# Optimization experiments

Hardware: AMD Instinct MI355X
Metric: run time of the kernel (lower is better)

## Reference

```python
import jax, jax.numpy as jnp
import numpy as np

B, S, E, H, W, HID, V, OUT, L = 2, 2048, 512, 8, 5, 2048, 32000, 6, 6
DH = E // H
SCALE = DH ** -0.5
PAD = (W - 1) // 2
SK = S - W + 1  # number of k/v windows from torch unfold


def setup_inputs() -> dict:
    key = jax.random.key(0)
    ks = jax.random.split(key, 16)
    def g(i, shape, s):
        return jax.random.normal(ks[i], shape, jnp.float32) * s
    return {
        "inputs": jax.random.randint(ks[0], (B, S), 0, V),
        "emb": g(1, (V, E), 0.02),
        "ln_w": jnp.ones((E,), jnp.float32),
        "ln_b": jnp.zeros((E,), jnp.float32),
        "q_w": g(2, (E, E), E ** -0.5), "q_b": jnp.zeros((E,), jnp.float32),
        "k_w": g(3, (E, E), E ** -0.5), "k_b": jnp.zeros((E,), jnp.float32),
        "v_w": g(4, (E, E), E ** -0.5), "v_b": jnp.zeros((E,), jnp.float32),
        "fc1_w": g(5, (E, HID), E ** -0.5), "fc1_b": jnp.zeros((HID,), jnp.float32),
        "fc2_w": g(6, (HID, E), HID ** -0.5), "fc2_b": jnp.zeros((E,), jnp.float32),
        "out_w": g(7, (E * S, OUT), (E * S) ** -0.5), "out_b": jnp.zeros((OUT,), jnp.float32),
    }


def _pos_encoding():
    pos = jnp.arange(S, dtype=jnp.float32)[:, None]
    div = jnp.exp(jnp.arange(0, E, 2, dtype=jnp.float32) * (-np.log(10000.0) / E))
    pe = jnp.zeros((S, E), jnp.float32)
    pe = pe.at[:, 0::2].set(jnp.sin(pos * div)).at[:, 1::2].set(jnp.cos(pos * div))
    return pe


def reference(inputs, emb, ln_w, ln_b, q_w, q_b, k_w, k_b, v_w, v_b,
              fc1_w, fc1_b, fc2_w, fc2_b, out_w, out_b):
    x = emb[inputs] + _pos_encoding()  # [B,S,E]

    def ln(t):
        m = t.mean(-1, keepdims=True)
        v_ = t.var(-1, keepdims=True)
        return (t - m) / jnp.sqrt(v_ + 1e-5) * ln_w + ln_b

    def attn(x):
        def heads(w, b):
            return (x @ w + b).reshape(B, S, H, DH).transpose(0, 2, 1, 3)  # [B,H,S,dh]
        q, k, v = heads(q_w, q_b), heads(k_w, k_b), heads(v_w, v_b)
        qp = jnp.pad(q, ((0, 0), (0, 0), (PAD, PAD), (0, 0)))  # [B,H,S+W-1,dh]
        # torch unfold -> windows [..., dh, W]; einsum contracts dh AND W, so flatten both.
        q_un = jnp.stack([qp[:, :, j:j + S, :] for j in range(W)], axis=-1).reshape(B, H, S, DH * W)
        k_un = jnp.stack([k[:, :, j:j + SK, :] for j in range(W)], axis=-1).reshape(B, H, SK, DH * W)
        scores = jnp.einsum('bhqf,bhkf->bhqk', q_un, k_un) * SCALE  # [B,H,S,SK]
        a = jax.nn.softmax(scores, axis=-1)
        # output einsum 'bnqk,bnkdh->bnqd' sums attn-weighted v over k AND window dim;
        # since attn is independent of window pos, presum v over the window.
        v_sum = sum(v[:, :, j:j + SK, :] for j in range(W))  # [B,H,SK,dh]
        o = jnp.einsum('bhqk,bhkd->bhqd', a, v_sum)
        return o.transpose(0, 2, 1, 3).reshape(B, S, E)

    for _ in range(L):
        x = ln(attn(x))
        x = (jax.nn.relu(x @ fc1_w + fc1_b) @ fc2_w + fc2_b) + x
        x = ln(x)
    return x.reshape(B, -1) @ out_w + out_b  # [B,OUT]
```

## Files before the change

kernel.cpp:

```cpp
#include <hip/hip_runtime.h>
#include <math.h>


namespace {
constexpr int kB   = 2;
constexpr int kS   = 2048;
constexpr int kE   = 512;
constexpr int kH   = 8;
constexpr int kDH  = 64;
constexpr int kSK  = 2044;
constexpr int kHID = 2048;
constexpr int kL   = 6;
constexpr float kScaleL2 = 0.125f * 1.44269504088896f;
constexpr int kTok = kB * kS;
constexpr int kNX  = kTok * kE;
constexpr int kQKV = 3 * kE;
constexpr int kSQ  = 72;
constexpr int kSV  = 136;
}

using f16x8   = __attribute__((ext_vector_type(8))) _Float16;
using floatx4 = __attribute__((ext_vector_type(4))) float;
using uint2v  = __attribute__((ext_vector_type(2))) unsigned int;
using uint4v  = __attribute__((ext_vector_type(4))) unsigned int;

static __device__ __forceinline__ unsigned short f2h(float f) {
  return __builtin_bit_cast(unsigned short, (_Float16)f);
}
static __device__ __forceinline__ float h2f(unsigned short u) {
  return (float)__builtin_bit_cast(_Float16, u);
}
static __device__ __forceinline__ unsigned int pk2h(float a, float b) {
  return __builtin_bit_cast(unsigned int, __builtin_amdgcn_cvt_pkrtz(a, b));
}
static __device__ __forceinline__ float red16(float x, bool hi) {
  const unsigned u = __builtin_bit_cast(unsigned, x);
  const uint2v r = __builtin_amdgcn_permlane16_swap(u, u, false, false);
  return __builtin_bit_cast(float, hi ? r[0] : r[1]);
}
static __device__ __forceinline__ float red32(float x, bool hi) {
  const unsigned u = __builtin_bit_cast(unsigned, x);
  const uint2v r = __builtin_amdgcn_permlane32_swap(u, u, false, false);
  return __builtin_bit_cast(float, hi ? r[0] : r[1]);
}

__global__ __launch_bounds__(256) void embed_kernel(const int* __restrict__ idx,
        const float* __restrict__ emb, unsigned short* __restrict__ X) {
  const int bs  = blockIdx.x;
  const int s   = bs & (kS - 1);
  const int tok = idx[bs];
  const int t   = threadIdx.x;
#pragma unroll
  for (int r = 0; r < 2; ++r) {
    const int e = t + 256 * r;
    const int i = e >> 1;
    const float dv  = __expf((float)(2 * i) * (-9.210340371976184f / (float)kE));
    const float ang = (float)s * dv;
    const float pe  = (e & 1) ? cosf(ang) : sinf(ang);
    X[bs * kE + e] = f2h(emb[tok * kE + e] + pe);
  }
}

__global__ __launch_bounds__(256) void tcast_kernel(const float* __restrict__ src,
        unsigned short* __restrict__ dst, int K, int N) {
  __shared__ float t[32][33];
  const int tid = threadIdx.x;
  const int tx = tid & 31, ty = tid >> 5;
  const int n0 = blockIdx.x * 32, k0 = blockIdx.y * 32;
#pragma unroll
  for (int p = 0; p < 4; ++p)
    t[ty + 8 * p][tx] = src[(size_t)(k0 + ty + 8 * p) * N + n0 + tx];
  __syncthreads();
#pragma unroll
  for (int p = 0; p < 4; ++p)
    dst[(size_t)(n0 + ty + 8 * p) * K + k0 + tx] = f2h(t[tx][ty + 8 * p]);
}

__global__ __launch_bounds__(256) void qkvb_kernel(const float* __restrict__ qb,
        const float* __restrict__ kb, const float* __restrict__ vb,
        float* __restrict__ dst) {
  const int i = blockIdx.x * 256 + threadIdx.x;
  dst[i] = (i < 512) ? qb[i] : ((i < 1024) ? kb[i - 512] : vb[i - 1024]);
}

template <int RELU, int RES>
__global__ __launch_bounds__(256) void mfma_gemm(const unsigned short* __restrict__ A,
        const unsigned short* __restrict__ Bt, const float* __restrict__ bias,
        const unsigned short* __restrict__ Rm, unsigned short* __restrict__ C,
        int M, int N, int K) {
  __shared__ __align__(16) unsigned short As[128 * 40];
  __shared__ __align__(16) unsigned short Bs[128 * 40];
  const int tid = threadIdx.x;
  const int m0 = blockIdx.y * 128, n0 = blockIdx.x * 128;
  const int wid = tid >> 6, lane = tid & 63;
  const int lm = lane & 15, quad = lane >> 4;
  const int wm = (wid & 1) * 64, wn = (wid >> 1) * 64;
  const int bn = tid >> 2, bk = (tid & 3) * 8;
  floatx4 acc[4][4] = {};
  for (int k0 = 0; k0 < K; k0 += 32) {
#pragma unroll
    for (int p = 0; p < 2; ++p) {
      const uint4 va = *(const uint4*)&A[(size_t)(m0 + bn + 64 * p) * K + k0 + bk];
      *(uint4*)&As[(bn + 64 * p) * 40 + bk] = va;
      const uint4 vb = *(const uint4*)&Bt[(size_t)(n0 + bn + 64 * p) * K + k0 + bk];
      *(uint4*)&Bs[(bn + 64 * p) * 40 + bk] = vb;
    }
    __syncthreads();
    f16x8 af[4], bf[4];
#pragma unroll
    for (int t = 0; t < 4; ++t) {
      af[t] = *(const f16x8*)&As[(wm + t * 16 + lm) * 40 + quad * 8];
      bf[t] = *(const f16x8*)&Bs[(wn + t * 16 + lm) * 40 + quad * 8];
    }
#pragma unroll
    for (int mt = 0; mt < 4; ++mt)
#pragma unroll
      for (int nt = 0; nt < 4; ++nt)
        acc[mt][nt] = __builtin_amdgcn_mfma_f32_16x16x32_f16(
            af[mt], bf[nt], acc[mt][nt], 0, 0, 0);
    __syncthreads();
  }
#pragma unroll
  for (int mt = 0; mt < 4; ++mt) {
#pragma unroll
    for (int nt = 0; nt < 4; ++nt) {
      const int n = n0 + wn + nt * 16 + lm;
      const float bv = bias[n];
#pragma unroll
      for (int r = 0; r < 4; ++r) {
        const int m = m0 + wm + mt * 16 + quad * 4 + r;
        float o = acc[mt][nt][r] + bv;
        if (RES) o += h2f(Rm[(size_t)m * N + n]);
        if (RELU) o = fmaxf(o, 0.f);
        C[(size_t)m * N + n] = f2h(o);
      }
    }
  }
}

__global__ __launch_bounds__(256) void vsumt_kernel(const unsigned short* __restrict__ QKVh,
        unsigned short* __restrict__ VsT) {
  const int t0 = blockIdx.x * 64;
  const int h = blockIdx.y, b = blockIdx.z;
  const int tid = threadIdx.x;
  __shared__ float Ls[68 * 65];
  for (int id = tid; id < 68 * 8; id += 256) {
    const int row = id >> 3, d8 = (id & 7) * 8;
    const int gt = t0 + row;
    float v[8];
    if (gt < kS) {
      const unsigned short* p =
          &QKVh[(size_t)(b * kS + gt) * kQKV + 2 * kE + h * kDH + d8];
      const ushort4 a = *(const ushort4*)p;
      const ushort4 c = *(const ushort4*)(p + 4);
      v[0] = h2f(a.x); v[1] = h2f(a.y); v[2] = h2f(a.z); v[3] = h2f(a.w);
      v[4] = h2f(c.x); v[5] = h2f(c.y); v[6] = h2f(c.z); v[7] = h2f(c.w);
    } else {
#pragma unroll
      for (int j = 0; j < 8; ++j) v[j] = 0.f;
    }
#pragma unroll
    for (int j = 0; j < 8; ++j) Ls[row * 65 + d8 + j] = v[j];
  }
  __syncthreads();
  const int t4 = (tid & 15) * 4;
#pragma unroll
  for (int c = 0; c < 4; ++c) {
    const int d = (tid >> 4) + 16 * c;
    ushort4 o;
    unsigned short* op = (unsigned short*)&o;
#pragma unroll
    for (int j = 0; j < 4; ++j) {
      const int tl = t4 + j;
      float s = Ls[(tl + 0) * 65 + d] + Ls[(tl + 1) * 65 + d]
              + Ls[(tl + 2) * 65 + d] + Ls[(tl + 3) * 65 + d]
              + Ls[(tl + 4) * 65 + d];
      if (t0 + tl >= kSK) s = 0.f;
      op[j] = f2h(s);
    }
    *(ushort4*)&VsT[((size_t)(b * kH + h) * kDH + d) * (size_t)kS + t0 + t4] = o;
  }
}

__global__ __launch_bounds__(512) void flash_kernel(const unsigned short* __restrict__ QKVh,
        const unsigned short* __restrict__ VsT, unsigned short* __restrict__ O) {
  const int tid = threadIdx.x;
  const int qt = blockIdx.x, h = blockIdx.y, b = blockIdx.z;
  const int q0 = qt * 64;
  const int wid = tid >> 6, lane = tid & 63;
  const int lm = lane & 15, quad = lane >> 4;
  const bool h16 = (lane & 16) != 0, h32 = (lane & 32) != 0;
  const int wq = wid >> 2, wt = wid & 3;
  const int bh = b * kH + h;

  __shared__ __align__(16) unsigned short Qs[68 * kSQ];
  __shared__ __align__(16) unsigned short Ks[132 * kSQ];
  __shared__ __align__(16) unsigned short Vt[64 * kSV];
  __shared__ float mM[64][4], lM[64][4];

  for (int id = tid; id < 68 * 16; id += 512) {
    const int row = id >> 4, c4 = (id & 15) * 4;
    const int gq = q0 - 2 + row;
    ushort4 v = make_ushort4(0, 0, 0, 0);
    if (gq >= 0 && gq < kS)
      v = *(const ushort4*)&QKVh[(size_t)(b * kS + gq) * kQKV + h * kDH + c4];
    *(ushort4*)&Qs[row * kSQ + c4] = v;
  }

  const int prow = tid >> 4;
  const int pc4 = (tid & 15) * 4, pc8 = (tid & 15) * 8;
  ushort4 kreg[5];
  uint4 vreg[2];
#define PREFETCH(T0)                                                          \
  {                                                                           \
    _Pragma("unroll")                                                         \
    for (int p = 0; p < 5; ++p) {                                             \
      const int row = prow + 32 * p;                                          \
      ushort4 v = make_ushort4(0, 0, 0, 0);                                   \
      if (row < 132) {                                                        \
        const int gk = (T0) + row;                                            \
        if (gk < kS)                                                          \
          v = *(const ushort4*)&QKVh[(size_t)(b * kS + gk) * kQKV + kE +      \
                                     h * kDH + pc4];                          \
      }                                                                       \
      kreg[p] = v;                                                            \
    }                                                                         \
    _Pragma("unroll")                                                         \
    for (int p = 0; p < 2; ++p)                                               \
      vreg[p] = *(const uint4*)&VsT[((size_t)bh * kDH + prow + 32 * p) *      \
                                    (size_t)kS + (T0) + pc8];                 \
  }
  PREFETCH(0)

  float mrow[2], lrow[2];
  mrow[0] = mrow[1] = -1e30f;
  lrow[0] = lrow[1] = 0.f;
  floatx4 Oacc[2][4] = {};
  const int asrc = (lane >> 2) & 12;

  for (int t0 = 0; t0 < kSK; t0 += 128) {
    __syncthreads();
#pragma unroll
    for (int p = 0; p < 5; ++p) {
      const int row = prow + 32 * p;
      if (row < 132) *(ushort4*)&Ks[row * kSQ + pc4] = kreg[p];
    }
#pragma unroll
    for (int p = 0; p < 2; ++p)
      *(uint4*)&Vt[(prow + 32 * p) * kSV + pc8] = vreg[p];
    __syncthreads();
    const int tn = t0 + 128;
    if (tn < kSK) PREFETCH(tn)

    floatx4 sac[2][2] = {};
    __builtin_amdgcn_s_setprio(1);
#pragma unroll
    for (int kk = 0; kk < 10; ++kk) {
      const int w = kk >> 1, d0 = (kk & 1) * 32;
      const f16x8 kf0 = *(const f16x8*)&Ks[(wt * 32 + lm + w) * kSQ + d0 + quad * 8];
      const f16x8 kf1 = *(const f16x8*)&Ks[(wt * 32 + 16 + lm + w) * kSQ + d0 + quad * 8];
      const f16x8 qf0 = *(const f16x8*)&Qs[(wq * 32 + lm + w) * kSQ + d0 + quad * 8];
      const f16x8 qf1 = *(const f16x8*)&Qs[(wq * 32 + 16 + lm + w) * kSQ + d0 + quad * 8];
      sac[0][0] = __builtin_amdgcn_mfma_f32_16x16x32_f16(kf0, qf0, sac[0][0], 0, 0, 0);
      sac[0][1] = __builtin_amdgcn_mfma_f32_16x16x32_f16(kf0, qf1, sac[0][1], 0, 0, 0);
      sac[1][0] = __builtin_amdgcn_mfma_f32_16x16x32_f16(kf1, qf0, sac[1][0], 0, 0, 0);
      sac[1][1] = __builtin_amdgcn_mfma_f32_16x16x32_f16(kf1, qf1, sac[1][1], 0, 0, 0);
    }
    __builtin_amdgcn_s_setprio(0);

    if (t0 + wt * 32 + 32 > kSK) {
#pragma unroll
      for (int tf = 0; tf < 2; ++tf)
#pragma unroll
        for (int r = 0; r < 4; ++r) {
          const int tg = t0 + wt * 32 + tf * 16 + quad * 4 + r;
          if (tg >= kSK) { sac[tf][0][r] = -1e30f; sac[tf][1][r] = -1e30f; }
        }
    }

    float alpha_q[2];
    f16x8 pfrag[2];
#pragma unroll
    for (int qf = 0; qf < 2; ++qf) {
      float mx = fmaxf(
          fmaxf(fmaxf(sac[0][qf][0], sac[0][qf][1]), fmaxf(sac[0][qf][2], sac[0][qf][3])),
          fmaxf(fmaxf(sac[1][qf][0], sac[1][qf][1]), fmaxf(sac[1][qf][2], sac[1][qf][3])));
      mx = fmaxf(mx, red16(mx, h16));
      mx = fmaxf(mx, red32(mx, h32));
      const float mnew = fmaxf(mrow[qf], mx * kScaleL2);
      const float al = exp2f(mrow[qf] - mnew);
      float e[2][4];
#pragma unroll
      for (int tf = 0; tf < 2; ++tf)
#pragma unroll
        for (int r = 0; r < 4; ++r)
          e[tf][r] = exp2f(fmaf(sac[tf][qf][r], kScaleL2, -mnew));
      float ps = ((e[0][0] + e[0][1]) + (e[0][2] + e[0][3]))
               + ((e[1][0] + e[1][1]) + (e[1][2] + e[1][3]));
      ps += red16(ps, h16);
      ps += red32(ps, h32);
      lrow[qf] = lrow[qf] * al + ps;
      mrow[qf] = mnew;
      alpha_q[qf] = al;
      const unsigned w00 = pk2h(e[0][0], e[0][1]);
      const unsigned w01 = pk2h(e[0][2], e[0][3]);
      const unsigned w10 = pk2h(e[1][0], e[1][1]);
      const unsigned w11 = pk2h(e[1][2], e[1][3]);
      const uint2v sA = __builtin_amdgcn_permlane32_swap(w00, w10, false, false);
      const uint2v dA = __builtin_amdgcn_permlane16_swap(sA[0], sA[1], false, false);
      const uint2v sB = __builtin_amdgcn_permlane32_swap(w01, w11, false, false);
      const uint2v dB = __builtin_amdgcn_permlane16_swap(sB[0], sB[1], false, false);
      uint4v fr;
      fr[0] = dA[0]; fr[1] = dB[0]; fr[2] = dA[1]; fr[3] = dB[1];
      pfrag[qf] = __builtin_bit_cast(f16x8, fr);
    }
    float alpha_o[2][4];
#pragma unroll
    for (int qf = 0; qf < 2; ++qf)
#pragma unroll
      for (int r = 0; r < 4; ++r)
        alpha_o[qf][r] = __shfl(alpha_q[qf], asrc + r);
#pragma unroll
    for (int ms = 0; ms < 2; ++ms)
#pragma unroll
      for (int nt2 = 0; nt2 < 4; ++nt2)
#pragma unroll
        for (int r = 0; r < 4; ++r)
          Oacc[ms][nt2][r] *= alpha_o[ms][r];
    {
      const int tcol = wt * 32 + quad * 8;
      __builtin_amdgcn_s_setprio(1);
#pragma unroll
      for (int nt2 = 0; nt2 < 4; ++nt2) {
        const f16x8 vf = *(const f16x8*)&Vt[(nt2 * 16 + lm) * kSV + tcol];
        Oacc[0][nt2] = __builtin_amdgcn_mfma_f32_16x16x32_f16(pfrag[0], vf, Oacc[0][nt2], 0, 0, 0);
        Oacc[1][nt2] = __builtin_amdgcn_mfma_f32_16x16x32_f16(pfrag[1], vf, Oacc[1][nt2], 0, 0, 0);
      }
      __builtin_amdgcn_s_setprio(0);
    }
  }
  if (quad == 0) {
#pragma unroll
    for (int qf = 0; qf < 2; ++qf) {
      const int row = wq * 32 + qf * 16 + lm;
      mM[row][wt] = mrow[qf];
      lM[row][wt] = lrow[qf];
    }
  }
  __syncthreads();
  float fac[2][4], invL[2][4];
#pragma unroll
  for (int qf = 0; qf < 2; ++qf)
#pragma unroll
    for (int r = 0; r < 4; ++r) {
      const int row = wq * 32 + qf * 16 + quad * 4 + r;
      const float M = fmaxf(fmaxf(mM[row][0], mM[row][1]),
                            fmaxf(mM[row][2], mM[row][3]));
      const float L = lM[row][0] * exp2f(mM[row][0] - M)
                    + lM[row][1] * exp2f(mM[row][1] - M)
                    + lM[row][2] * exp2f(mM[row][2] - M)
                    + lM[row][3] * exp2f(mM[row][3] - M);
      fac[qf][r] = exp2f(mM[row][wt] - M);
      invL[qf][r] = 1.f / L;
    }
  float* OfA = (float*)Vt;
  float* OfB = (float*)Ks;
  if (!(wt & 1)) {
    float* Of = (wt == 0) ? OfA : OfB;
#pragma unroll
    for (int ms = 0; ms < 2; ++ms)
#pragma unroll
      for (int nt2 = 0; nt2 < 4; ++nt2)
#pragma unroll
        for (int r = 0; r < 4; ++r)
          Of[(wq * 32 + ms * 16 + quad * 4 + r) * 68 + nt2 * 16 + lm] =
              Oacc[ms][nt2][r] * fac[ms][r];
  }
  __syncthreads();
  if (wt & 1) {
    float* Of = (wt == 1) ? OfA : OfB;
#pragma unroll
    for (int ms = 0; ms < 2; ++ms)
#pragma unroll
      for (int nt2 = 0; nt2 < 4; ++nt2)
#pragma unroll
        for (int r = 0; r < 4; ++r)
          Of[(wq * 32 + ms * 16 + quad * 4 + r) * 68 + nt2 * 16 + lm] +=
              Oacc[ms][nt2][r] * fac[ms][r];
  }
  __syncthreads();
  if (wt == 0) {
#pragma unroll
    for (int ms = 0; ms < 2; ++ms)
#pragma unroll
      for (int r = 0; r < 4; ++r) {
        const int row = wq * 32 + ms * 16 + quad * 4 + r;
        const int q = q0 + row;
#pragma unroll
        for (int nt2 = 0; nt2 < 4; ++nt2) {
          const float o = (OfA[row * 68 + nt2 * 16 + lm]
                           + OfB[row * 68 + nt2 * 16 + lm]) * invL[ms][r];
          O[(size_t)(b * kS + q) * kE + h * kDH + nt2 * 16 + lm] = f2h(o);
        }
      }
  }
}

__global__ __launch_bounds__(256) void ln_kernel(const unsigned short* __restrict__ Xin,
        const float* __restrict__ w, const float* __restrict__ bb,
        unsigned short* __restrict__ Y) {
  const int row = blockIdx.x;
  const int tid = threadIdx.x;
  const unsigned short* xr = Xin + (size_t)row * kE;
  const ushort2 vv = *(const ushort2*)&xr[tid * 2];
  const float v0 = h2f(vv.x), v1 = h2f(vv.y);
  float s = v0 + v1, sq = v0 * v0 + v1 * v1;
  for (int off = 32; off; off >>= 1) {
    s  += __shfl_down(s, off);
    sq += __shfl_down(sq, off);
  }
  __shared__ float rs[4], rq[4];
  const int wid = tid >> 6;
  if ((tid & 63) == 0) { rs[wid] = s; rq[wid] = sq; }
  __syncthreads();
  const float St = rs[0] + rs[1] + rs[2] + rs[3];
  const float Qt = rq[0] + rq[1] + rq[2] + rq[3];
  const float mean = St * (1.f / kE);
  const float var  = Qt * (1.f / kE) - mean * mean;
  const float rstd = rsqrtf(var + 1e-5f);
  const float2 wv = *(const float2*)&w[tid * 2];
  const float2 bv = *(const float2*)&bb[tid * 2];
  ushort2 o;
  o.x = f2h((v0 - mean) * rstd * wv.x + bv.x);
  o.y = f2h((v1 - mean) * rstd * wv.y + bv.y);
  *(ushort2*)&(Y + (size_t)row * kE)[tid * 2] = o;
}

__global__ __launch_bounds__(256) void final_kernel(const unsigned short* __restrict__ X,
        const float* __restrict__ Wt, const float* __restrict__ bias,
        float* __restrict__ out) {
  const int b = blockIdx.y, chunk = blockIdx.x;
  const int tid = threadIdx.x;
  const unsigned short* xb = X + (size_t)b * (kS * kE);
  float acc[6] = {};
  const int k0 = chunk * 8192;
#pragma unroll 4
  for (int i = 0; i < 32; ++i) {
    const int kk = k0 + tid + i * 256;
    const float xv = h2f(xb[kk]);
    const float* wr = Wt + (size_t)kk * 6;
#pragma unroll
    for (int o = 0; o < 6; ++o) acc[o] = fmaf(xv, wr[o], acc[o]);
  }
#pragma unroll
  for (int o = 0; o < 6; ++o)
    for (int off = 32; off; off >>= 1) acc[o] += __shfl_down(acc[o], off);
  __shared__ float part[4][6];
  const int wid = tid >> 6;
  if ((tid & 63) == 0) {
#pragma unroll
    for (int o = 0; o < 6; ++o) part[wid][o] = acc[o];
  }
  __syncthreads();
  if (tid < 6) {
    float s2 = part[0][tid] + part[1][tid] + part[2][tid] + part[3][tid];
    if (chunk == 0) s2 += bias[tid];
    atomicAdd(&out[b * 6 + tid], s2);
  }
}

extern "C" void kernel_launch(void* const* d_in, const int* in_sizes, int n_in,
                              void* d_out, int out_size, void* d_ws, size_t ws_size,
                              hipStream_t stream) {
  (void)in_sizes; (void)n_in; (void)ws_size;
  const int*   tok   = (const int*)d_in[0];
  const float* emb   = (const float*)d_in[1];
  const float* ln_w  = (const float*)d_in[2];
  const float* ln_b  = (const float*)d_in[3];
  const float* q_w   = (const float*)d_in[4];
  const float* q_b   = (const float*)d_in[5];
  const float* k_w   = (const float*)d_in[6];
  const float* k_b   = (const float*)d_in[7];
  const float* v_w   = (const float*)d_in[8];
  const float* v_b   = (const float*)d_in[9];
  const float* fc1_w = (const float*)d_in[10];
  const float* fc1_b = (const float*)d_in[11];
  const float* fc2_w = (const float*)d_in[12];
  const float* fc2_b = (const float*)d_in[13];
  const float* out_w = (const float*)d_in[14];
  const float* out_b = (const float*)d_in[15];

  float* ws = (float*)d_ws;
  unsigned short* x16 = (unsigned short*)ws;
  unsigned short* y16 = (unsigned short*)(ws + (size_t)kNX / 2);
  float* regA = ws + (size_t)kNX;
  unsigned short* qkvh = (unsigned short*)regA;
  unsigned short* hbuf = (unsigned short*)regA;
  unsigned short* wqkvT = (unsigned short*)(ws + (size_t)3 * kNX);
  unsigned short* fc1T  = wqkvT + (size_t)kQKV * kE;
  unsigned short* fc2T  = fc1T + (size_t)kHID * kE;
  float* qkvb = (float*)(fc2T + (size_t)kE * kHID);
  unsigned short* vsT = (unsigned short*)(qkvb + kQKV);

  tcast_kernel<<<dim3(16, 16), 256, 0, stream>>>(q_w, wqkvT, kE, kE);
  tcast_kernel<<<dim3(16, 16), 256, 0, stream>>>(k_w, wqkvT + (size_t)kE * kE, kE, kE);
  tcast_kernel<<<dim3(16, 16), 256, 0, stream>>>(v_w, wqkvT + (size_t)2 * kE * kE, kE, kE);
  tcast_kernel<<<dim3(64, 16), 256, 0, stream>>>(fc1_w, fc1T, kE, kHID);
  tcast_kernel<<<dim3(16, 64), 256, 0, stream>>>(fc2_w, fc2T, kHID, kE);
  qkvb_kernel<<<dim3(6), 256, 0, stream>>>(q_b, k_b, v_b, qkvb);

  embed_kernel<<<dim3(kTok), 256, 0, stream>>>(tok, emb, x16);
  for (int l = 0; l < kL; ++l) {
    mfma_gemm<0, 0><<<dim3(kQKV / 128, kTok / 128), 256, 0, stream>>>(
        x16, wqkvT, qkvb, nullptr, qkvh, kTok, kQKV, kE);
    vsumt_kernel<<<dim3(kS / 64, kH, kB), 256, 0, stream>>>(qkvh, vsT);
    flash_kernel<<<dim3(kS / 64, kH, kB), 512, 0, stream>>>(qkvh, vsT, y16);
    ln_kernel<<<dim3(kTok), 256, 0, stream>>>(y16, ln_w, ln_b, x16);
    mfma_gemm<1, 0><<<dim3(kHID / 128, kTok / 128), 256, 0, stream>>>(
        x16, fc1T, fc1_b, nullptr, hbuf, kTok, kHID, kE);
    mfma_gemm<0, 1><<<dim3(kE / 128, kTok / 128), 256, 0, stream>>>(
        hbuf, fc2T, fc2_b, x16, y16, kTok, kE, kHID);
    ln_kernel<<<dim3(kTok), 256, 0, stream>>>(y16, ln_w, ln_b, x16);
  }
  hipMemsetAsync(d_out, 0, (size_t)out_size * sizeof(float), stream);
  final_kernel<<<dim3(128, kB), 256, 0, stream>>>(x16, out_w, out_b, (float*)d_out);
}
```

Measured before the change: 1.249 ms.

## Prefetch GEMM tiles into registers, skip lazy softmax rescale, wave-per-row layernorm

The GEMM now loads the next K-slice from global memory into registers while MFMAs run on the current LDS tile, and raises wave priority around the MFMA block. The flash kernel skips the output rescale when the running max grows by no more than 8 (log2 units) across the wave, which saves shuffles and multiplies. It risks fp16 overflow headroom in P. LayerNorm now handles one row per wavefront with 8-element vector loads and no LDS reduction or block barrier.

```diff
diff --git a/kernel.cpp b/kernel.cpp
--- a/kernel.cpp
+++ b/kernel.cpp
@@ -96,29 +96,43 @@
   const int lm = lane & 15, quad = lane >> 4;
   const int wm = (wid & 1) * 64, wn = (wid >> 1) * 64;
   const int bn = tid >> 2, bk = (tid & 3) * 8;
+  uint4 pa[2], pb[2];
+#pragma unroll
+  for (int p = 0; p < 2; ++p) {
+    pa[p] = *(const uint4*)&A[(size_t)(m0 + bn + 64 * p) * K + bk];
+    pb[p] = *(const uint4*)&Bt[(size_t)(n0 + bn + 64 * p) * K + bk];
+  }
   floatx4 acc[4][4] = {};
   for (int k0 = 0; k0 < K; k0 += 32) {
+    __syncthreads();
 #pragma unroll
     for (int p = 0; p < 2; ++p) {
-      const uint4 va = *(const uint4*)&A[(size_t)(m0 + bn + 64 * p) * K + k0 + bk];
-      *(uint4*)&As[(bn + 64 * p) * 40 + bk] = va;
-      const uint4 vb = *(const uint4*)&Bt[(size_t)(n0 + bn + 64 * p) * K + k0 + bk];
-      *(uint4*)&Bs[(bn + 64 * p) * 40 + bk] = vb;
+      *(uint4*)&As[(bn + 64 * p) * 40 + bk] = pa[p];
+      *(uint4*)&Bs[(bn + 64 * p) * 40 + bk] = pb[p];
     }
     __syncthreads();
+    const int kn = k0 + 32;
+    if (kn < K) {
+#pragma unroll
+      for (int p = 0; p < 2; ++p) {
+        pa[p] = *(const uint4*)&A[(size_t)(m0 + bn + 64 * p) * K + kn + bk];
+        pb[p] = *(const uint4*)&Bt[(size_t)(n0 + bn + 64 * p) * K + kn + bk];
+      }
+    }
     f16x8 af[4], bf[4];
 #pragma unroll
     for (int t = 0; t < 4; ++t) {
       af[t] = *(const f16x8*)&As[(wm + t * 16 + lm) * 40 + quad * 8];
       bf[t] = *(const f16x8*)&Bs[(wn + t * 16 + lm) * 40 + quad * 8];
     }
+    __builtin_amdgcn_s_setprio(1);
 #pragma unroll
     for (int mt = 0; mt < 4; ++mt)
 #pragma unroll
       for (int nt = 0; nt < 4; ++nt)
         acc[mt][nt] = __builtin_amdgcn_mfma_f32_16x16x32_f16(
             af[mt], bf[nt], acc[mt][nt], 0, 0, 0);
-    __syncthreads();
+    __builtin_amdgcn_s_setprio(0);
   }
 #pragma unroll
   for (int mt = 0; mt < 4; ++mt) {
@@ -279,6 +293,7 @@
     }
 
     float alpha_q[2];
+    int skip_q[2];
     f16x8 pfrag[2];
 #pragma unroll
     for (int qf = 0; qf < 2; ++qf) {
@@ -287,8 +302,11 @@
           fmaxf(fmaxf(sac[1][qf][0], sac[1][qf][1]), fmaxf(sac[1][qf][2], sac[1][qf][3])));
       mx = fmaxf(mx, red16(mx, h16));
       mx = fmaxf(mx, red32(mx, h32));
-      const float mnew = fmaxf(mrow[qf], mx * kScaleL2);
-      const float al = exp2f(mrow[qf] - mnew);
+      const float mxs = mx * kScaleL2;
+      const int skip = __all(mxs <= mrow[qf] + 8.f);
+      float mnew, al;
+      if (skip) { mnew = mrow[qf]; al = 1.f; }
+      else      { mnew = fmaxf(mrow[qf], mxs); al = exp2f(mrow[qf] - mnew); }
       float e[2][4];
 #pragma unroll
       for (int tf = 0; tf < 2; ++tf)
@@ -302,6 +320,7 @@
       lrow[qf] = lrow[qf] * al + ps;
       mrow[qf] = mnew;
       alpha_q[qf] = al;
+      skip_q[qf] = skip;
       const unsigned w00 = pk2h(e[0][0], e[0][1]);
       const unsigned w01 = pk2h(e[0][2], e[0][3]);
       const unsigned w10 = pk2h(e[1][0], e[1][1]);
@@ -314,19 +333,21 @@
       fr[0] = dA[0]; fr[1] = dB[0]; fr[2] = dA[1]; fr[3] = dB[1];
       pfrag[qf] = __builtin_bit_cast(f16x8, fr);
     }
-    float alpha_o[2][4];
-#pragma unroll
-    for (int qf = 0; qf < 2; ++qf)
-#pragma unroll
-      for (int r = 0; r < 4; ++r)
-        alpha_o[qf][r] = __shfl(alpha_q[qf], asrc + r);
-#pragma unroll
-    for (int ms = 0; ms < 2; ++ms)
-#pragma unroll
-      for (int nt2 = 0; nt2 < 4; ++nt2)
+    if (!(skip_q[0] && skip_q[1])) {
+      float alpha_o[2][4];
+#pragma unroll
+      for (int qf = 0; qf < 2; ++qf)
 #pragma unroll
         for (int r = 0; r < 4; ++r)
-          Oacc[ms][nt2][r] *= alpha_o[ms][r];
+          alpha_o[qf][r] = __shfl(alpha_q[qf], asrc + r);
+#pragma unroll
+      for (int ms = 0; ms < 2; ++ms)
+#pragma unroll
+        for (int nt2 = 0; nt2 < 4; ++nt2)
+#pragma unroll
+          for (int r = 0; r < 4; ++r)
+            Oacc[ms][nt2][r] *= alpha_o[ms][r];
+    }
     {
       const int tcol = wt * 32 + quad * 8;
       __builtin_amdgcn_s_setprio(1);
@@ -409,31 +430,40 @@
 __global__ __launch_bounds__(256) void ln_kernel(const unsigned short* __restrict__ Xin,
         const float* __restrict__ w, const float* __restrict__ bb,
         unsigned short* __restrict__ Y) {
-  const int row = blockIdx.x;
-  const int tid = threadIdx.x;
-  const unsigned short* xr = Xin + (size_t)row * kE;
-  const ushort2 vv = *(const ushort2*)&xr[tid * 2];
-  const float v0 = h2f(vv.x), v1 = h2f(vv.y);
-  float s = v0 + v1, sq = v0 * v0 + v1 * v1;
+  const int wid = threadIdx.x >> 6, lane = threadIdx.x & 63;
+  const int row = blockIdx.x * 4 + wid;
+  const unsigned short* xr = Xin + (size_t)row * kE + lane * 8;
+  const ushort4 a = *(const ushort4*)xr;
+  const ushort4 c = *(const ushort4*)(xr + 4);
+  float v[8] = { h2f(a.x), h2f(a.y), h2f(a.z), h2f(a.w),
+                 h2f(c.x), h2f(c.y), h2f(c.z), h2f(c.w) };
+  float s = 0.f, sq = 0.f;
+#pragma unroll
+  for (int j = 0; j < 8; ++j) { s += v[j]; sq += v[j] * v[j]; }
+#pragma unroll
   for (int off = 32; off; off >>= 1) {
-    s  += __shfl_down(s, off);
-    sq += __shfl_down(sq, off);
-  }
-  __shared__ float rs[4], rq[4];
-  const int wid = tid >> 6;
-  if ((tid & 63) == 0) { rs[wid] = s; rq[wid] = sq; }
-  __syncthreads();
-  const float St = rs[0] + rs[1] + rs[2] + rs[3];
-  const float Qt = rq[0] + rq[1] + rq[2] + rq[3];
-  const float mean = St * (1.f / kE);
-  const float var  = Qt * (1.f / kE) - mean * mean;
+    s  += __shfl_xor(s, off);
+    sq += __shfl_xor(sq, off);
+  }
+  const float mean = s * (1.f / kE);
+  const float var  = sq * (1.f / kE) - mean * mean;
   const float rstd = rsqrtf(var + 1e-5f);
-  const float2 wv = *(const float2*)&w[tid * 2];
-  const float2 bv = *(const float2*)&bb[tid * 2];
-  ushort2 o;
-  o.x = f2h((v0 - mean) * rstd * wv.x + bv.x);
-  o.y = f2h((v1 - mean) * rstd * wv.y + bv.y);
-  *(ushort2*)&(Y + (size_t)row * kE)[tid * 2] = o;
+  const float4 w0 = *(const float4*)&w[lane * 8];
+  const float4 w1 = *(const float4*)&w[lane * 8 + 4];
+  const float4 b0 = *(const float4*)&bb[lane * 8];
+  const float4 b1 = *(const float4*)&bb[lane * 8 + 4];
+  const float wa[8] = { w0.x, w0.y, w0.z, w0.w, w1.x, w1.y, w1.z, w1.w };
+  const float ba[8] = { b0.x, b0.y, b0.z, b0.w, b1.x, b1.y, b1.z, b1.w };
+  ushort4 o0, o1;
+  unsigned short* op = (unsigned short*)&o0;
+#pragma unroll
+  for (int j = 0; j < 4; ++j) op[j] = f2h((v[j] - mean) * rstd * wa[j] + ba[j]);
+  op = (unsigned short*)&o1;
+#pragma unroll
+  for (int j = 0; j < 4; ++j) op[j] = f2h((v[4 + j] - mean) * rstd * wa[4 + j] + ba[4 + j]);
+  unsigned short* yr = Y + (size_t)row * kE + lane * 8;
+  *(ushort4*)yr = o0;
+  *(ushort4*)(yr + 4) = o1;
 }
 
 __global__ __launch_bounds__(256) void final_kernel(const unsigned short* __restrict__ X,
@@ -515,12 +545,12 @@
         x16, wqkvT, qkvb, nullptr, qkvh, kTok, kQKV, kE);
     vsumt_kernel<<<dim3(kS / 64, kH, kB), 256, 0, stream>>>(qkvh, vsT);
     flash_kernel<<<dim3(kS / 64, kH, kB), 512, 0, stream>>>(qkvh, vsT, y16);
-    ln_kernel<<<dim3(kTok), 256, 0, stream>>>(y16, ln_w, ln_b, x16);
+    ln_kernel<<<dim3(kTok / 4), 256, 0, stream>>>(y16, ln_w, ln_b, x16);
     mfma_gemm<1, 0><<<dim3(kHID / 128, kTok / 128), 256, 0, stream>>>(
         x16, fc1T, fc1_b, nullptr, hbuf, kTok, kHID, kE);
     mfma_gemm<0, 1><<<dim3(kE / 128, kTok / 128), 256, 0, stream>>>(
         hbuf, fc2T, fc2_b, x16, y16, kTok, kE, kHID);
-    ln_kernel<<<dim3(kTok), 256, 0, stream>>>(y16, ln_w, ln_b, x16);
+    ln_kernel<<<dim3(kTok / 4), 256, 0, stream>>>(y16, ln_w, ln_b, x16);
   }
   hipMemsetAsync(d_out, 0, (size_t)out_size * sizeof(float), stream);
   final_kernel<<<dim3(128, kB), 256, 0, stream>>>(x16, out_w, out_b, (float*)d_out);
```

Measured after the change: 1.759 ms. 1.41x slower.
